# Kernel optimization log

Hardware: AMD Instinct MI355X
Metric: run time of the kernel (lower is better)

## Reference

```python
import jax, jax.numpy as jnp
import numpy as np

NUM_IN_CAPS = 1152   # 32 * 6 * 6
NUM_OUT_CAPS = 10
IN_DIM = 8
OUT_DIM = 16
ROUTING_ITERS = 3
EPS = 1e-8


def squash(s, axis=-1):
    # squash(s) = ||s||^2/(1+||s||^2) * s/||s||
    sq = jnp.sum(s * s, axis=axis, keepdims=True)
    norm = jnp.sqrt(sq + EPS)
    return (sq / (1.0 + sq)) * (s / norm)


def setup_inputs() -> dict:
    key = jax.random.key(0)
    ks = jax.random.split(key, 6)
    B = 512
    inp = jax.random.uniform(ks[0], (B, 1, 28, 28), dtype=jnp.float32)
    # conv params (He-ish scale)
    conv1_w = jax.random.normal(ks[1], (256, 1, 9, 9), dtype=jnp.float32) * 0.05
    conv1_b = jnp.zeros((256,), dtype=jnp.float32)
    conv2_w = jax.random.normal(ks[2], (256, 256, 9, 9), dtype=jnp.float32) * 0.01
    conv2_b = jnp.zeros((256,), dtype=jnp.float32)
    # capsule transform weights: [in_caps, out_caps, in_dim, out_dim]
    cap_W = jax.random.normal(ks[3], (NUM_IN_CAPS, NUM_OUT_CAPS, IN_DIM, OUT_DIM), dtype=jnp.float32) * 0.05
    return {"input": inp, "conv1_w": conv1_w, "conv1_b": conv1_b,
            "conv2_w": conv2_w, "conv2_b": conv2_b, "cap_W": cap_W}


def _conv(x, w, b, stride):
    y = jax.lax.conv_general_dilated(
        x, w, window_strides=(stride, stride), padding='VALID',
        dimension_numbers=('NCHW', 'OIHW', 'NCHW'))
    return y + b[None, :, None, None]


def capsnet_forward(input, conv1_w, conv1_b, conv2_w, conv2_b, cap_W):
    B = input.shape[0]
    h = jax.nn.relu(_conv(input, conv1_w, conv1_b, 1))   # [B,256,20,20]
    h = _conv(h, conv2_w, conv2_b, 2)                    # [B,256,6,6]
    # torch.transpose(output, 1, -1): [B,C,H,W] -> [B,W,H,C], then view(B,1152,8)
    u = jnp.transpose(h, (0, 3, 2, 1)).reshape(B, NUM_IN_CAPS, IN_DIM)
    # predicted output vectors u_hat: [B, i, j, q]
    u_hat = jnp.einsum('bip,ijpq->bijq', u, cap_W)
    # dynamic routing
    b_ij = jnp.zeros((B, NUM_IN_CAPS, NUM_OUT_CAPS), dtype=u_hat.dtype)
    v = None
    for _ in range(ROUTING_ITERS):
        c = jax.nn.softmax(b_ij, axis=2)                 # coupling over output caps
        s = jnp.einsum('bij,bijq->bjq', c, u_hat)        # [B, j, q]
        v = squash(s)                                    # [B, j, q]
        b_ij = b_ij + jnp.einsum('bijq,bjq->bij', u_hat, v)
    return v  # [B, 10, 16]


def reference(input, conv1_w, conv1_b, conv2_w, conv2_b, cap_W):
    return capsnet_forward(input, conv1_w, conv1_b, conv2_w, conv2_b, cap_W)
```

## Files before the change

kernel.cpp:

```cpp
#include <hip/hip_runtime.h>
#include <hip/hip_bf16.h>

typedef __attribute__((ext_vector_type(8))) short bf16x8;
typedef __attribute__((ext_vector_type(4))) float f32x4;

static __device__ __forceinline__ unsigned short f2bf(float x) {
    __hip_bfloat16 h = __float2bfloat16(x);
    return *(unsigned short*)&h;
}
static __device__ __forceinline__ float bflo(unsigned int w) { return __uint_as_float(w << 16); }
static __device__ __forceinline__ float bfhi(unsigned int w) { return __uint_as_float(w & 0xffff0000u); }
static __device__ __forceinline__ float bf1(unsigned short u) { return __uint_as_float(((unsigned int)u) << 16); }

typedef __attribute__((address_space(1))) const void gvoid;
typedef __attribute__((address_space(3))) void lvoid;
static __device__ __forceinline__ void gl_lds16(const void* g, void* l) {
    __builtin_amdgcn_global_load_lds((gvoid*)g, (lvoid*)l, 16, 0, 0);
}

#define PART_FLOATS 4718592

__global__ __launch_bounds__(320) void conv1_k(const float* __restrict__ in,
                                               const float* __restrict__ w,
                                               const float* __restrict__ bias,
                                               unsigned short* __restrict__ h1n) {
    int blk = blockIdx.x;
    int b = blk >> 4;
    int c0 = (blk & 15) * 16;
    __shared__ float img[784];
    __shared__ float wl[16 * 81];
    __shared__ float bl[16];
    __shared__ unsigned short tr[20 * 328];
    int tid = threadIdx.x;
    for (int t = tid; t < 784; t += 320) img[t] = in[b * 784 + t];
    for (int t = tid; t < 1296; t += 320) wl[t] = w[c0 * 81 + t];
    if (tid < 16) bl[tid] = bias[c0 + tid];
    __syncthreads();

    int co = tid / 20, oy = tid % 20;
    float wr[81];
#pragma unroll
    for (int k = 0; k < 81; k++) wr[k] = wl[co * 81 + k];
    float acc[20];
    float bv = bl[co];
#pragma unroll
    for (int ox = 0; ox < 20; ox++) acc[ox] = bv;

#pragma unroll
    for (int ky = 0; ky < 9; ky++) {
        const float* rp = &img[(oy + ky) * 28];
        float r[28];
#pragma unroll
        for (int v = 0; v < 7; v++) {
            float4 t4 = ((const float4*)rp)[v];
            r[v * 4 + 0] = t4.x; r[v * 4 + 1] = t4.y;
            r[v * 4 + 2] = t4.z; r[v * 4 + 3] = t4.w;
        }
#pragma unroll
        for (int kx = 0; kx < 9; kx++) {
            float wv = wr[ky * 9 + kx];
#pragma unroll
            for (int ox = 0; ox < 20; ox++) acc[ox] += r[ox + kx] * wv;
        }
    }
#pragma unroll
    for (int ox = 0; ox < 20; ox++)
        tr[oy * 328 + ox * 16 + co] = f2bf(fmaxf(acc[ox], 0.f));
    __syncthreads();
    for (int g = tid; g < 800; g += 320) {
        int p = g >> 1, half = g & 1;
        uint4 v = *(uint4*)&tr[(p / 20) * 328 + (p % 20) * 16 + half * 8];
        *(uint4*)&h1n[(b * 400 + p) * 256 + c0 + half * 8] = v;
    }
}

__global__ __launch_bounds__(256) void wt2_k(const float* __restrict__ w2,
                                             unsigned short* __restrict__ Wt2) {
    int cout = blockIdx.x;
    int ci = threadIdx.x;
    const float* src = w2 + (cout * 256 + ci) * 81;
#pragma unroll 1
    for (int kk = 0; kk < 81; kk++)
        Wt2[kk * 65536 + cout * 256 + ci] = f2bf(src[kk]);
#pragma unroll
    for (int kk = 81; kk < 84; kk++)
        Wt2[kk * 65536 + cout * 256 + ci] = 0;
}

__global__ __launch_bounds__(256) void conv2_k(const unsigned short* __restrict__ h1n,
                                               const unsigned short* __restrict__ Wt2,
                                               const float* __restrict__ bias,
                                               float* __restrict__ u,
                                               float* __restrict__ part1,
                                               float* __restrict__ part23) {
    __shared__ unsigned short sA[2][128 * 64];
    __shared__ unsigned short sB[2][128 * 64];
    int tid = threadIdx.x;
    int m0 = blockIdx.x * 128;
    int n0 = blockIdx.y * 128;
    int slice = blockIdx.z;
    int ks = slice * 21;

    int wv = tid >> 6, lane = tid & 63;
    int wm = wv >> 1, wn = wv & 1;
    int lr = lane & 15, quad = lane >> 4;

    int lrow = lane >> 3, lslot = lane & 7;
    int kcoff = (lslot ^ lrow) * 8;
    int aG[4], bG[4];
#pragma unroll
    for (int t = 0; t < 4; t++) {
        int r = wv * 32 + t * 8 + lrow;
        int R = m0 + r;
        int b = R / 36, m = R % 36;
        int oy = m / 6, ox = m % 6;
        aG[t] = b * 102400 + oy * 10240 + ox * 512 + kcoff;
        bG[t] = (n0 + r) * 256 + kcoff;
    }

    f32x4 acc[4][4];
#pragma unroll
    for (int i = 0; i < 4; i++)
#pragma unroll
        for (int j = 0; j < 4; j++) acc[i][j] = (f32x4){0.f, 0.f, 0.f, 0.f};

    auto stage = [&](int buf, int rr) {
        int kk = ks + (rr >> 2), cr = rr & 3;
        int ky = kk / 9, kx = kk % 9;
        int aoff = ky * 5120 + kx * 256 + cr * 64;
        int boff = kk * 65536 + cr * 64;
        unsigned short* dA = &sA[buf][wv * 2048];
        unsigned short* dB = &sB[buf][wv * 2048];
#pragma unroll
        for (int t = 0; t < 4; t++)
            gl_lds16(h1n + aG[t] + aoff, dA + t * 512);
#pragma unroll
        for (int t = 0; t < 4; t++)
            gl_lds16(Wt2 + bG[t] + boff, dB + t * 512);
    };

    stage(0, 0);
    __syncthreads();

    int cur = 0;
#pragma unroll 1
    for (int rr = 0; rr < 84; rr++) {
        if (rr < 83) stage(cur ^ 1, rr + 1);
        const unsigned short* pA = &sA[cur][0];
        const unsigned short* pB = &sB[cur][0];
#pragma unroll
        for (int s = 0; s < 2; s++) {
            bf16x8 af[4], bf[4];
#pragma unroll
            for (int i = 0; i < 4; i++) {
                int arow = wm * 64 + i * 16 + lr;
                af[i] = *(bf16x8*)&pA[arow * 64 + 8 * ((s * 4 + quad) ^ (lr & 7))];
            }
#pragma unroll
            for (int j = 0; j < 4; j++) {
                int brow = wn * 64 + j * 16 + lr;
                bf[j] = *(bf16x8*)&pB[brow * 64 + 8 * ((s * 4 + quad) ^ (lr & 7))];
            }
#pragma unroll
            for (int i = 0; i < 4; i++)
#pragma unroll
                for (int j = 0; j < 4; j++)
                    acc[i][j] = __builtin_amdgcn_mfma_f32_16x16x32_bf16(
                        af[i], bf[j], acc[i][j], 0, 0, 0);
        }
        __syncthreads();
        cur ^= 1;
    }

    float* dst = (slice == 0) ? u : ((slice == 1) ? part1 : part23 + (size_t)(slice - 2) * PART_FLOATS);
#pragma unroll
    for (int j = 0; j < 4; j++) {
        int col = n0 + wn * 64 + j * 16 + lr;
        float bv = (slice == 0) ? bias[col] : 0.f;
#pragma unroll
        for (int i = 0; i < 4; i++) {
#pragma unroll
            for (int rg = 0; rg < 4; rg++) {
                int RR = m0 + wm * 64 + i * 16 + quad * 4 + rg;
                int bb = RR / 36, mm = RR % 36;
                int oyy = mm / 6, oxx = mm % 6;
                dst[bb * 9216 + oxx * 1536 + oyy * 256 + col] = acc[i][j][rg] + bv;
            }
        }
    }
}

__global__ __launch_bounds__(256) void add_k(float* __restrict__ u,
                                             const float* __restrict__ p1,
                                             const float* __restrict__ p23) {
    int n = (blockIdx.x * 256 + threadIdx.x) * 4;
    float4 a = *(float4*)&u[n];
    float4 x = *(const float4*)&p1[n];
    float4 y = *(const float4*)&p23[n];
    float4 z = *(const float4*)&p23[PART_FLOATS + n];
    a.x += x.x + y.x + z.x;
    a.y += x.y + y.y + z.y;
    a.z += x.z + y.z + z.z;
    a.w += x.w + y.w + z.w;
    *(float4*)&u[n] = a;
}

__global__ __launch_bounds__(256) void uhat_k(const float* __restrict__ u,
                                              const float* __restrict__ W,
                                              unsigned short* __restrict__ uhat) {
    int i0 = blockIdx.x * 64;
    int b0 = blockIdx.y * 8;
    __shared__ float ul[8 * 64 * 9];
    __shared__ float wl[64 * 129];
    int tid = threadIdx.x;

    for (int t = tid; t < 4096; t += 256) {
        int bb = t >> 9, r = t & 511;
        ul[bb * 576 + (r >> 3) * 9 + (r & 7)] = u[(b0 + bb) * 9216 + i0 * 8 + r];
    }

    int il = tid & 63, g = tid >> 6;
    for (int j = 0; j < 10; j++) {
        __syncthreads();
        for (int t = tid; t < 2048; t += 256) {
            int li = t >> 5, off = (t & 31) * 4;
            float4 v = *(const float4*)&W[(i0 + li) * 1280 + j * 128 + off];
            float* d = &wl[li * 129 + off];
            d[0] = v.x; d[1] = v.y; d[2] = v.z; d[3] = v.w;
        }
        __syncthreads();
#pragma unroll 1
        for (int bb = 0; bb < 8; bb++) {
            float ur[8];
#pragma unroll
            for (int p = 0; p < 8; p++) ur[p] = ul[bb * 576 + il * 9 + p];
            float a[4];
#pragma unroll
            for (int k = 0; k < 4; k++) {
                int q = g * 4 + k;
                float s = 0.f;
#pragma unroll
                for (int p = 0; p < 8; p++) s += ur[p] * wl[il * 129 + p * 16 + q];
                a[k] = s;
            }
            unsigned int lo = (unsigned int)f2bf(a[0]) | ((unsigned int)f2bf(a[1]) << 16);
            unsigned int hi = (unsigned int)f2bf(a[2]) | ((unsigned int)f2bf(a[3]) << 16);
            uint2 pk; pk.x = lo; pk.y = hi;
            *(uint2*)&uhat[((size_t)(b0 + bb) * 10 + j) * 18432 + (size_t)(i0 + il) * 16 + g * 4] = pk;
        }
    }
}

__global__ __launch_bounds__(256) void route_k(const unsigned short* __restrict__ uhat,
                                               float* __restrict__ out) {
    int b = blockIdx.x;
    int tid = threadIdx.x;
    int w = tid >> 6, lane = tid & 63;
    int ig = lane >> 2, qh = lane & 3;
    __shared__ float b_sh[1152 * 10];
    __shared__ float s_red[4 * 160];
    __shared__ float v_sh[160];
    __shared__ float sc_sh[10];
    const unsigned short* ub = uhat + (size_t)b * 184320;

    float v_ln[10][4];

    auto finish = [&](float sp[10][4]) {
#pragma unroll
        for (int j = 0; j < 10; j++)
#pragma unroll
            for (int k = 0; k < 4; k++) {
                float t = sp[j][k];
                t += __shfl_xor(t, 4);
                t += __shfl_xor(t, 8);
                t += __shfl_xor(t, 16);
                t += __shfl_xor(t, 32);
                sp[j][k] = t;
            }
        if (ig == 0) {
#pragma unroll
            for (int j = 0; j < 10; j++) {
                f32x4 v4 = {sp[j][0], sp[j][1], sp[j][2], sp[j][3]};
                *(f32x4*)&s_red[w * 160 + j * 16 + qh * 4] = v4;
            }
        }
        __syncthreads();
        if (tid < 160) {
            float s = s_red[tid] + s_red[160 + tid] + s_red[320 + tid] + s_red[480 + tid];
            s_red[tid] = s;
        }
        __syncthreads();
        if (tid < 10) {
            float sq = 0.f;
#pragma unroll
            for (int q = 0; q < 16; q++) { float x = s_red[tid * 16 + q]; sq += x * x; }
            float norm = sqrtf(sq + 1e-8f);
            sc_sh[tid] = (sq / (1.0f + sq)) / norm;
        }
        __syncthreads();
        if (tid < 160) v_sh[tid] = s_red[tid] * sc_sh[tid >> 4];
        __syncthreads();
#pragma unroll
        for (int j = 0; j < 10; j++) {
            f32x4 v4 = *(const f32x4*)&v_sh[j * 16 + qh * 4];
            v_ln[j][0] = v4[0]; v_ln[j][1] = v4[1]; v_ln[j][2] = v4[2]; v_ln[j][3] = v4[3];
        }
        __syncthreads();
    };

    {
        float sp[10][4];
#pragma unroll
        for (int j = 0; j < 10; j++)
#pragma unroll
            for (int k = 0; k < 4; k++) sp[j][k] = 0.f;
#pragma unroll 2
        for (int r = 0; r < 18; r++) {
            int i = r * 64 + w * 16 + ig;
            const unsigned short* up = ub + (size_t)i * 16 + qh * 4;
            uint2 uh[10];
#pragma unroll
            for (int j = 0; j < 10; j++) uh[j] = *(const uint2*)(up + (size_t)j * 18432);
#pragma unroll
            for (int j = 0; j < 10; j++) {
                sp[j][0] += 0.1f * bflo(uh[j].x);
                sp[j][1] += 0.1f * bfhi(uh[j].x);
                sp[j][2] += 0.1f * bflo(uh[j].y);
                sp[j][3] += 0.1f * bfhi(uh[j].y);
            }
        }
        finish(sp);
    }

#pragma unroll 1
    for (int pass = 0; pass < 2; pass++) {
        bool first = (pass == 0);
        float sp[10][4];
#pragma unroll
        for (int j = 0; j < 10; j++)
#pragma unroll
            for (int k = 0; k < 4; k++) sp[j][k] = 0.f;
#pragma unroll 2
        for (int r = 0; r < 18; r++) {
            int i = r * 64 + w * 16 + ig;
            const unsigned short* up = ub + (size_t)i * 16 + qh * 4;
            uint2 uh[10];
#pragma unroll
            for (int j = 0; j < 10; j++) uh[j] = *(const uint2*)(up + (size_t)j * 18432);
            float d[10];
#pragma unroll
            for (int j = 0; j < 10; j++) {
                d[j] = bflo(uh[j].x) * v_ln[j][0] + bfhi(uh[j].x) * v_ln[j][1]
                     + bflo(uh[j].y) * v_ln[j][2] + bfhi(uh[j].y) * v_ln[j][3];
            }
#pragma unroll
            for (int j = 0; j < 10; j++) {
                d[j] += __shfl_xor(d[j], 1);
                d[j] += __shfl_xor(d[j], 2);
            }
            float bn[10];
            if (first) {
#pragma unroll
                for (int j = 0; j < 10; j++) bn[j] = d[j];
#pragma unroll
                for (int j = 0; j < 10; j++)
                    if (qh == (j & 3)) b_sh[i * 10 + j] = bn[j];
            } else {
#pragma unroll
                for (int j = 0; j < 10; j++) bn[j] = b_sh[i * 10 + j] + d[j];
            }
            float m = bn[0];
#pragma unroll
            for (int j = 1; j < 10; j++) m = fmaxf(m, bn[j]);
            float e[10], sum = 0.f;
#pragma unroll
            for (int j = 0; j < 10; j++) { e[j] = __expf(bn[j] - m); sum += e[j]; }
            float inv = 1.f / sum;
#pragma unroll
            for (int j = 0; j < 10; j++) {
                float c = e[j] * inv;
                sp[j][0] += c * bflo(uh[j].x);
                sp[j][1] += c * bfhi(uh[j].x);
                sp[j][2] += c * bflo(uh[j].y);
                sp[j][3] += c * bfhi(uh[j].y);
            }
        }
        finish(sp);
    }

    if (tid < 160) out[b * 160 + tid] = v_sh[tid];
}

extern "C" void kernel_launch(void* const* d_in, const int* in_sizes, int n_in,
                              void* d_out, int out_size, void* d_ws, size_t ws_size,
                              hipStream_t stream) {
    const float* input = (const float*)d_in[0];
    const float* c1w = (const float*)d_in[1];
    const float* c1b = (const float*)d_in[2];
    const float* c2w = (const float*)d_in[3];
    const float* c2b = (const float*)d_in[4];
    const float* capW = (const float*)d_in[5];
    float* out = (float*)d_out;

    const size_t U_OFF = 0;
    const size_t L_OFF = 19529728;
    const size_t B_OFF = 43122688;
    const size_t WT2_BYTES = (size_t)84 * 65536 * 2;
    const size_t H1N_BYTES = 104857600;
    const size_t PART_BYTES = (size_t)PART_FLOATS * 4;
    const size_t CONV_BYTES = WT2_BYTES + H1N_BYTES + 2 * PART_BYTES;
    if (ws_size < B_OFF + CONV_BYTES) return;

    char* wsb = (char*)d_ws;
    float* u_buf = (float*)(wsb + U_OFF);
    float* part1  = (float*)(wsb + L_OFF);
    unsigned short* Wt2 = (unsigned short*)(wsb + B_OFF);
    unsigned short* h1n = (unsigned short*)(wsb + B_OFF + WT2_BYTES);
    float* part23 = (float*)(wsb + B_OFF + WT2_BYTES + H1N_BYTES);
    unsigned short* uhatb = (unsigned short*)(wsb + B_OFF);

    size_t availB = ws_size - B_OFF;
    int Cr = 0;
    const int cands[7] = {512, 256, 128, 64, 32, 16, 8};
    for (int k = 0; k < 7; k++) {
        if ((size_t)cands[k] * 368640 <= availB) { Cr = cands[k]; break; }
    }
    if (Cr == 0) return;

    wt2_k<<<256, 256, 0, stream>>>(c2w, Wt2);
    conv1_k<<<512 * 16, 320, 0, stream>>>(input, c1w, c1b, h1n);
    conv2_k<<<dim3(144, 2, 4), 256, 0, stream>>>(h1n, Wt2, c2b, u_buf, part1, part23);
    add_k<<<4608, 256, 0, stream>>>(u_buf, part1, part23);

    for (int b0 = 0; b0 < 512; b0 += Cr) {
        uhat_k<<<dim3(18, Cr / 8), 256, 0, stream>>>(u_buf + (size_t)b0 * 9216, capW,
                                                     uhatb + (size_t)b0 * 184320);
        route_k<<<Cr, 256, 0, stream>>>(uhatb + (size_t)b0 * 184320, out + (size_t)b0 * 160);
    }
}
```

Baseline: 744.1 us.

## Load conv2 weight fragments directly into registers instead of staging through LDS

The B operand (conv2 weights) of the conv2 GEMM no longer goes through shared memory. Each wave loads its MFMA B fragments straight from global memory into double-buffered registers, while A keeps its LDS double buffer. The main loop is unrolled by two so the register buffers alternate. This halves LDS traffic and footprint but raises register pressure, and each wave now issues uncoalesced 16-byte global loads of weights that were shared across waves in the same block.

Result: slower. 971.5 us (+30.6%).

```diff
diff --git a/kernel.cpp b/kernel.cpp
--- a/kernel.cpp
+++ b/kernel.cpp
@@ -94,7 +94,6 @@
                                                float* __restrict__ part1,
                                                float* __restrict__ part23) {
     __shared__ unsigned short sA[2][128 * 64];
-    __shared__ unsigned short sB[2][128 * 64];
     int tid = threadIdx.x;
     int m0 = blockIdx.x * 128;
     int n0 = blockIdx.y * 128;
@@ -107,7 +106,7 @@
 
     int lrow = lane >> 3, lslot = lane & 7;
     int kcoff = (lslot ^ lrow) * 8;
-    int aG[4], bG[4];
+    int aG[4];
 #pragma unroll
     for (int t = 0; t < 4; t++) {
         int r = wv * 32 + t * 8 + lrow;
@@ -115,8 +114,14 @@
         int b = R / 36, m = R % 36;
         int oy = m / 6, ox = m % 6;
         aG[t] = b * 102400 + oy * 10240 + ox * 512 + kcoff;
-        bG[t] = (n0 + r) * 256 + kcoff;
-    }
+    }
+
+    int bL[2][4];
+#pragma unroll
+    for (int s = 0; s < 2; s++)
+#pragma unroll
+        for (int j = 0; j < 4; j++)
+            bL[s][j] = (n0 + wn * 64 + j * 16 + lr) * 256 + (s * 4 + quad) * 8;
 
     f32x4 acc[4][4];
 #pragma unroll
@@ -124,52 +129,58 @@
 #pragma unroll
         for (int j = 0; j < 4; j++) acc[i][j] = (f32x4){0.f, 0.f, 0.f, 0.f};
 
-    auto stage = [&](int buf, int rr) {
+    auto stageA = [&](int buf, int rr) {
         int kk = ks + (rr >> 2), cr = rr & 3;
-        int ky = kk / 9, kx = kk % 9;
-        int aoff = ky * 5120 + kx * 256 + cr * 64;
-        int boff = kk * 65536 + cr * 64;
+        int aoff = (kk / 9) * 5120 + (kk % 9) * 256 + cr * 64;
         unsigned short* dA = &sA[buf][wv * 2048];
-        unsigned short* dB = &sB[buf][wv * 2048];
 #pragma unroll
         for (int t = 0; t < 4; t++)
             gl_lds16(h1n + aG[t] + aoff, dA + t * 512);
-#pragma unroll
-        for (int t = 0; t < 4; t++)
-            gl_lds16(Wt2 + bG[t] + boff, dB + t * 512);
     };
 
-    stage(0, 0);
-    __syncthreads();
-
-    int cur = 0;
-#pragma unroll 1
-    for (int rr = 0; rr < 84; rr++) {
-        if (rr < 83) stage(cur ^ 1, rr + 1);
-        const unsigned short* pA = &sA[cur][0];
-        const unsigned short* pB = &sB[cur][0];
+    bf16x8 rB0[2][4], rB1[2][4];
+    auto loadB = [&](bf16x8 (&rB)[2][4], int rr) {
+        int kk = ks + (rr >> 2), cr = rr & 3;
+        int boff = kk * 65536 + cr * 64;
+#pragma unroll
+        for (int s = 0; s < 2; s++)
+#pragma unroll
+            for (int j = 0; j < 4; j++)
+                rB[s][j] = *(const bf16x8*)(Wt2 + boff + bL[s][j]);
+    };
+
+    auto compute = [&](const unsigned short* pA, bf16x8 (&rB)[2][4]) {
 #pragma unroll
         for (int s = 0; s < 2; s++) {
-            bf16x8 af[4], bf[4];
+            bf16x8 af[4];
 #pragma unroll
             for (int i = 0; i < 4; i++) {
                 int arow = wm * 64 + i * 16 + lr;
                 af[i] = *(bf16x8*)&pA[arow * 64 + 8 * ((s * 4 + quad) ^ (lr & 7))];
             }
 #pragma unroll
-            for (int j = 0; j < 4; j++) {
-                int brow = wn * 64 + j * 16 + lr;
-                bf[j] = *(bf16x8*)&pB[brow * 64 + 8 * ((s * 4 + quad) ^ (lr & 7))];
-            }
-#pragma unroll
             for (int i = 0; i < 4; i++)
 #pragma unroll
                 for (int j = 0; j < 4; j++)
                     acc[i][j] = __builtin_amdgcn_mfma_f32_16x16x32_bf16(
-                        af[i], bf[j], acc[i][j], 0, 0, 0);
-        }
-        __syncthreads();
-        cur ^= 1;
+                        af[i], rB[s][j], acc[i][j], 0, 0, 0);
+        }
+    };
+
+    loadB(rB0, 0);
+    stageA(0, 0);
+    __syncthreads();
+
+#pragma unroll 1
+    for (int it = 0; it < 42; it++) {
+        int rr = it * 2;
+        loadB(rB1, rr + 1);
+        stageA(1, rr + 1);
+        compute(&sA[0][0], rB0);
+        __syncthreads();
+        if (rr + 2 < 84) { loadB(rB0, rr + 2); stageA(0, rr + 2); }
+        compute(&sA[1][0], rB1);
+        __syncthreads();
     }
 
     float* dst = (slice == 0) ? u : ((slice == 1) ? part1 : part23 + (size_t)(slice - 2) * PART_FLOATS);
```

## Fuse split-K partial reduction into uhat kernel and use bf16 capsule weights

Applied to the files above, without the earlier changes.

Removes the separate add_k pass: uhat_k now sums the four split-K conv2 partial buffers while loading u into shared memory. Capsule weights are pre-converted to bf16 by a new kernel, which halves weight traffic and shared-memory footprint in uhat_k. The batch tile per block goes from 8 to 16, and routing runs in two fixed 256-sample chunks that reuse one uhat buffer. The cost is an extra conversion launch, bf16 rounding of the capsule weights, and a fixed chunk count instead of one sized to the available workspace.

Measured after the change: 814.8 us. +9.5%, slower.

```diff
diff --git a/kernel.cpp b/kernel.cpp
--- a/kernel.cpp
+++ b/kernel.cpp
@@ -87,6 +87,16 @@
         Wt2[kk * 65536 + cout * 256 + ci] = 0;
 }
 
+__global__ __launch_bounds__(256) void wcap_k(const float* __restrict__ W,
+                                              unsigned short* __restrict__ Wb) {
+    int idx4 = blockIdx.x * 256 + threadIdx.x;
+    float4 v = *(const float4*)&W[(size_t)idx4 * 4];
+    unsigned int lo = (unsigned int)f2bf(v.x) | ((unsigned int)f2bf(v.y) << 16);
+    unsigned int hi = (unsigned int)f2bf(v.z) | ((unsigned int)f2bf(v.w) << 16);
+    uint2 pk; pk.x = lo; pk.y = hi;
+    *(uint2*)&Wb[(size_t)idx4 * 4] = pk;
+}
+
 __global__ __launch_bounds__(256) void conv2_k(const unsigned short* __restrict__ h1n,
                                                const unsigned short* __restrict__ Wt2,
                                                const float* __restrict__ bias,
@@ -190,47 +200,35 @@
     }
 }
 
-__global__ __launch_bounds__(256) void add_k(float* __restrict__ u,
-                                             const float* __restrict__ p1,
-                                             const float* __restrict__ p23) {
-    int n = (blockIdx.x * 256 + threadIdx.x) * 4;
-    float4 a = *(float4*)&u[n];
-    float4 x = *(const float4*)&p1[n];
-    float4 y = *(const float4*)&p23[n];
-    float4 z = *(const float4*)&p23[PART_FLOATS + n];
-    a.x += x.x + y.x + z.x;
-    a.y += x.y + y.y + z.y;
-    a.z += x.z + y.z + z.z;
-    a.w += x.w + y.w + z.w;
-    *(float4*)&u[n] = a;
-}
-
 __global__ __launch_bounds__(256) void uhat_k(const float* __restrict__ u,
-                                              const float* __restrict__ W,
+                                              const float* __restrict__ p1,
+                                              const float* __restrict__ p23,
+                                              const unsigned short* __restrict__ Wb,
                                               unsigned short* __restrict__ uhat) {
     int i0 = blockIdx.x * 64;
-    int b0 = blockIdx.y * 8;
-    __shared__ float ul[8 * 64 * 9];
-    __shared__ float wl[64 * 129];
+    int b0 = blockIdx.y * 16;
+    __shared__ float ul[16 * 576];
+    __shared__ unsigned short wl[64 * 130];
     int tid = threadIdx.x;
 
-    for (int t = tid; t < 4096; t += 256) {
+    for (int t = tid; t < 8192; t += 256) {
         int bb = t >> 9, r = t & 511;
-        ul[bb * 576 + (r >> 3) * 9 + (r & 7)] = u[(b0 + bb) * 9216 + i0 * 8 + r];
+        int gidx = (b0 + bb) * 9216 + i0 * 8 + r;
+        float v = u[gidx] + p1[gidx] + p23[gidx] + p23[PART_FLOATS + gidx];
+        ul[bb * 576 + (r >> 3) * 9 + (r & 7)] = v;
     }
 
     int il = tid & 63, g = tid >> 6;
     for (int j = 0; j < 10; j++) {
         __syncthreads();
-        for (int t = tid; t < 2048; t += 256) {
-            int li = t >> 5, off = (t & 31) * 4;
-            float4 v = *(const float4*)&W[(i0 + li) * 1280 + j * 128 + off];
-            float* d = &wl[li * 129 + off];
-            d[0] = v.x; d[1] = v.y; d[2] = v.z; d[3] = v.w;
+        for (int t = tid; t < 4096; t += 256) {
+            int li = t >> 6, cp = t & 63;
+            *(unsigned int*)&wl[li * 130 + cp * 2] =
+                *(const unsigned int*)&Wb[(size_t)(i0 + li) * 1280 + j * 128 + cp * 2];
         }
         __syncthreads();
 #pragma unroll 1
-        for (int bb = 0; bb < 8; bb++) {
+        for (int bb = 0; bb < 16; bb++) {
             float ur[8];
 #pragma unroll
             for (int p = 0; p < 8; p++) ur[p] = ul[bb * 576 + il * 9 + p];
@@ -240,7 +238,7 @@
                 int q = g * 4 + k;
                 float s = 0.f;
 #pragma unroll
-                for (int p = 0; p < 8; p++) s += ur[p] * wl[il * 129 + p * 16 + q];
+                for (int p = 0; p < 8; p++) s += ur[p] * bf1(wl[il * 130 + p * 16 + q]);
                 a[k] = s;
             }
             unsigned int lo = (unsigned int)f2bf(a[0]) | ((unsigned int)f2bf(a[1]) << 16);
@@ -403,7 +401,8 @@
     float* out = (float*)d_out;
 
     const size_t U_OFF = 0;
-    const size_t L_OFF = 19529728;
+    const size_t P1_OFF = 18874368;
+    const size_t WB_OFF = 37748736;
     const size_t B_OFF = 43122688;
     const size_t WT2_BYTES = (size_t)84 * 65536 * 2;
     const size_t H1N_BYTES = 104857600;
@@ -413,28 +412,23 @@
 
     char* wsb = (char*)d_ws;
     float* u_buf = (float*)(wsb + U_OFF);
-    float* part1  = (float*)(wsb + L_OFF);
+    float* part1 = (float*)(wsb + P1_OFF);
+    unsigned short* Wb = (unsigned short*)(wsb + WB_OFF);
     unsigned short* Wt2 = (unsigned short*)(wsb + B_OFF);
     unsigned short* h1n = (unsigned short*)(wsb + B_OFF + WT2_BYTES);
     float* part23 = (float*)(wsb + B_OFF + WT2_BYTES + H1N_BYTES);
     unsigned short* uhatb = (unsigned short*)(wsb + B_OFF);
 
-    size_t availB = ws_size - B_OFF;
-    int Cr = 0;
-    const int cands[7] = {512, 256, 128, 64, 32, 16, 8};
-    for (int k = 0; k < 7; k++) {
-        if ((size_t)cands[k] * 368640 <= availB) { Cr = cands[k]; break; }
-    }
-    if (Cr == 0) return;
-
+    wcap_k<<<1440, 256, 0, stream>>>(capW, Wb);
     wt2_k<<<256, 256, 0, stream>>>(c2w, Wt2);
     conv1_k<<<512 * 16, 320, 0, stream>>>(input, c1w, c1b, h1n);
     conv2_k<<<dim3(144, 2, 4), 256, 0, stream>>>(h1n, Wt2, c2b, u_buf, part1, part23);
-    add_k<<<4608, 256, 0, stream>>>(u_buf, part1, part23);
-
+
+    const int Cr = 256;
     for (int b0 = 0; b0 < 512; b0 += Cr) {
-        uhat_k<<<dim3(18, Cr / 8), 256, 0, stream>>>(u_buf + (size_t)b0 * 9216, capW,
-                                                     uhatb + (size_t)b0 * 184320);
-        route_k<<<Cr, 256, 0, stream>>>(uhatb + (size_t)b0 * 184320, out + (size_t)b0 * 160);
-    }
-}
+        uhat_k<<<dim3(18, Cr / 16), 256, 0, stream>>>(
+            u_buf + (size_t)b0 * 9216, part1 + (size_t)b0 * 9216,
+            part23 + (size_t)b0 * 9216, Wb, uhatb);
+        route_k<<<Cr, 256, 0, stream>>>(uhatb, out + (size_t)b0 * 160);
+    }
+}
```
